# Kernel optimization log

Measured on AMD Instinct MI355X. Metric: run time of the kernel, lower is better.

Reference implementation:

```python
import jax, jax.numpy as jnp
import numpy as np

B = 2048        # patients (segments)
K = 4           # images per patient
C = 1280        # backbone_out (tf_efficientnet_b0)
PAIRS = K * (K - 1) // 2  # torch.combinations -> 6
NCLS = 1
N_DROP = 5


def setup_inputs() -> dict:
    key = jax.random.key(0)
    ks = jax.random.split(key, 8)
    x = jax.random.normal(ks[0], (B * K, C), jnp.float32)  # detached backbone features
    ids2 = jnp.repeat(jnp.arange(B, dtype=jnp.int32), PAIRS)  # segment id per pair
    Wc = jax.random.normal(ks[1], (C, C, 2), jnp.float32) * 0.02  # Conv1d(C,C,k=2) weight
    bc = jnp.zeros((C,), jnp.float32)
    W0 = jax.random.normal(ks[2], (NCLS, C), jnp.float32) * 0.02
    b0 = jnp.zeros((NCLS,), jnp.float32)
    W1 = jax.random.normal(ks[3], (1, C), jnp.float32) * 0.02
    b1 = jnp.zeros((1,), jnp.float32)
    W2 = jax.random.normal(ks[4], (1, C), jnp.float32) * 0.02
    b2 = jnp.zeros((1,), jnp.float32)
    return dict(x=x, ids2=ids2, Wc=Wc, bc=bc, W0=W0, b0=b0, W1=W1, b1=b1, W2=W2, b2=b2)


def reference(x, ids2, Wc, bc, W0, b0, W1, b1, W2, b2):
    # --- pair combinations within each patient group of K images ---
    ii, jj = np.triu_indices(K, 1)               # static [PAIRS]
    xg = x.reshape(B, K, C)
    xa = xg[:, ii].reshape(B * PAIRS, C)         # first element of each pair
    xb = xg[:, jj].reshape(B * PAIRS, C)         # second element
    # Conv1d(C, C, kernel=2) over the length-2 pair sequence + ReLU
    xc = jax.nn.relu(xa @ Wc[:, :, 0].T + xb @ Wc[:, :, 1].T + bc)  # [P, C]

    # --- 5 fixed dropout masks (p=0.5, train-mode scaling) ---
    masks = jax.random.bernoulli(jax.random.key(42), 0.5,
                                 (N_DROP, xc.shape[0], C)).astype(xc.dtype) * 2.0
    xd = xc[None] * masks                        # [D, P, C]

    cnt = jax.ops.segment_sum(jnp.ones_like(ids2, dtype=xc.dtype),
                              ids2, num_segments=B)  # [B], == PAIRS

    def agg(W, b):
        # head -> scalar mean over classes -> segment-mean over pairs -> mean over dropouts
        z = (jnp.einsum('dpc,oc->dpo', xd, W) + b).mean(-1)          # [D, P]
        s = jax.vmap(lambda u: jax.ops.segment_sum(u, ids2, num_segments=B))(z)
        return (s / cnt).mean(0)                                      # [B]

    logits = agg(W0, b0)
    logits1 = agg(W1, b1)
    logits2 = agg(W2, b2)
    return jnp.stack([logits, logits1, logits2], axis=1)  # [B, 3]
```

## Files before the change

kernel.cpp:

```cpp
#include <hip/hip_runtime.h>


typedef __attribute__((ext_vector_type(8))) short short8;
typedef __attribute__((ext_vector_type(4))) float f32x4;

#define PLANE 15728640u
#define KS2   (0x1BD11BDAu ^ 42u)

__device__ __forceinline__ unsigned short f2bf(float f) {
  unsigned int u = __builtin_bit_cast(unsigned int, f);
  u = (u + 0x7FFFu + ((u >> 16) & 1u)) >> 16;
  return (unsigned short)u;
}
__device__ __forceinline__ float bf2f(unsigned short h) {
  unsigned int u = ((unsigned int)h) << 16;
  return __builtin_bit_cast(float, u);
}

__global__ __launch_bounds__(256) void prep(
    const float* __restrict__ x, unsigned short* __restrict__ xb,
    const float* __restrict__ Wc, unsigned short* __restrict__ Wb,
    const float* __restrict__ b0, const float* __restrict__ b1,
    const float* __restrict__ b2, float* __restrict__ out) {
  const int bid = blockIdx.x;
  const int t = threadIdx.x;
  if (bid < 10240) {
    const int i = (bid * 256 + t) * 4;
    float4 v = *(const float4*)(x + i);
    ushort4 o;
    o.x = f2bf(v.x); o.y = f2bf(v.y); o.z = f2bf(v.z); o.w = f2bf(v.w);
    *(ushort4*)(xb + i) = o;
  } else if (bid < 23040) {
    const int idx = (bid - 10240) * 256 + t;
    const int n = idx / 2560;
    const int k = idx - n * 2560;
    const int side = (k >= 1280) ? 1 : 0;
    const int cin = k - side * 1280;
    Wb[idx] = f2bf(Wc[n * 2560 + cin * 2 + side]);
  } else {
    const int i = (bid - 23040) * 256 + t;
    if (i < 2048 * 3) {
      const int h = i % 3;
      out[i] = (h == 0) ? b0[0] : ((h == 1) ? b1[0] : b2[0]);
    }
  }
}

__device__ __forceinline__ unsigned int rotl(unsigned int x, int r) {
  return __builtin_amdgcn_alignbit(x, x, 32 - r);
}
__device__ __forceinline__ unsigned int tf_msb(unsigned int x1) {
  unsigned int x0 = x1;
  x1 = rotl(x1, 13) ^ x0;
#define TF_R(r) { x0 += x1; x1 = rotl(x1, (r)) ^ x0; }
  TF_R(15) TF_R(26) TF_R(6)
  x0 += 42u; x1 += KS2 + 1u;
  TF_R(17) TF_R(29) TF_R(16) TF_R(24)
  x0 += KS2; x1 += 2u;
  TF_R(13) TF_R(15) TF_R(26) TF_R(6)
  x1 += 42u + 3u;
  TF_R(17) TF_R(29) TF_R(16) TF_R(24)
  x0 += 42u; x1 += KS2 + 4u;
  TF_R(13) TF_R(15) TF_R(26) TF_R(6)
  x0 += KS2; x1 += 5u;
#undef TF_R
  return (x0 ^ x1) >> 31;
}

#define GL_LDS(g, l) __builtin_amdgcn_global_load_lds( \
    (const __attribute__((address_space(1))) unsigned int*)(g), \
    (__attribute__((address_space(3))) unsigned int*)(l), 16, 0, 0)

__global__ __launch_bounds__(256) void gemm_relu_dot(
    const unsigned short* __restrict__ Xb,
    const unsigned short* __restrict__ Wb,
    const float* __restrict__ bc,
    const float* __restrict__ W0, const float* __restrict__ W1,
    const float* __restrict__ W2, float* __restrict__ out)
{
  __shared__ unsigned short sA[2 * 128 * 32];
  __shared__ unsigned short sB[2 * 128 * 32];
  __shared__ unsigned int zLDS[8 * 256];
  __shared__ float rowsumA[128 * 3];
  __shared__ float rowsumB[128 * 3];

  const int t = threadIdx.x;
  const int mblk = blockIdx.x % 96;
  const int nblk = blockIdx.x / 96;
  const int p0 = mblk * 128, n0 = nblk * 128;
  const int lane = t & 63, w = t >> 6;
  const int wr = w >> 1, wc = w & 1;
  const int q = lane & 3;
  const int rl = lane >> 2;
  const int mrow = lane & 15;
  const int koff = (lane >> 4) * 8;
  const int mq = (lane >> 4) * 4;
  const int nn = lane & 15;

  int rA[2], rB[2], rN[2];
#pragma unroll
  for (int i = 0; i < 2; i++) {
    const int row = w * 32 + i * 16 + rl;
    const int pg = p0 + row;
    const int bA = pg / 6, pr = pg - bA * 6;
    rA[i] = bA * 4 + ((0x211000 >> (4 * pr)) & 7);
    rB[i] = bA * 4 + ((0x332321 >> (4 * pr)) & 7);
    rN[i] = n0 + row;
  }
  unsigned short* const ldsA0 = sA + (w * 32 + 0) * 32;
  unsigned short* const ldsA1 = sA + (w * 32 + 16) * 32;
  unsigned short* const ldsB0 = sB + (w * 32 + 0) * 32;
  unsigned short* const ldsB1 = sB + (w * 32 + 16) * 32;
  const unsigned short* const gA0s0 = Xb + rA[0] * 1280 + q * 8;
  const unsigned short* const gA1s0 = Xb + rA[1] * 1280 + q * 8;
  const unsigned short* const gA0s1 = Xb + rB[0] * 1280 + q * 8;
  const unsigned short* const gA1s1 = Xb + rB[1] * 1280 + q * 8;
  const unsigned short* const gB0 = Wb + rN[0] * 2560 + q * 8;
  const unsigned short* const gB1 = Wb + rN[1] * 2560 + q * 8;

  f32x4 acc[4][4];
#pragma unroll
  for (int i = 0; i < 4; i++)
#pragma unroll
    for (int j = 0; j < 4; j++) acc[i][j] = (f32x4){0.f, 0.f, 0.f, 0.f};

  const unsigned int tb =
      (unsigned int)((p0 + wr * 64 + mq) * 1280 + n0 + wc * 64 + nn) + 42u;

#define PF(nxt, bb)                                                          \
  {                                                                          \
    const int _n = (nxt);                                                    \
    if (_n < 80) {                                                           \
      const int _s1 = (_n >= 40);                                            \
      const unsigned short* _a0 = _s1 ? gA0s1 : gA0s0;                       \
      const unsigned short* _a1 = _s1 ? gA1s1 : gA1s0;                       \
      const int _kb = (_s1 ? (_n - 40) : _n) * 32;                           \
      const int _kg = _n * 32;                                               \
      GL_LDS(_a0 + _kb, ldsA0 + (bb) * 4096);                                \
      GL_LDS(_a1 + _kb, ldsA1 + (bb) * 4096);                                \
      GL_LDS(gB0 + _kg, ldsB0 + (bb) * 4096);                                \
      GL_LDS(gB1 + _kg, ldsB1 + (bb) * 4096);                                \
    }                                                                        \
  }

#define KSTEP(it, bb)                                                        \
  {                                                                          \
    __syncthreads();                                                         \
    short8 af[4], bfr[4];                                                    \
    _Pragma("unroll")                                                        \
    for (int i = 0; i < 4; i++)                                              \
      af[i] = *(const short8*)(sA + (bb) * 4096 +                            \
                               (wr * 64 + i * 16 + mrow) * 32 + koff);       \
    _Pragma("unroll")                                                        \
    for (int j = 0; j < 4; j++)                                              \
      bfr[j] = *(const short8*)(sB + (bb) * 4096 +                           \
                                (wc * 64 + j * 16 + mrow) * 32 + koff);      \
    PF((it) + 1, ((bb) ^ 1));                                                \
    _Pragma("unroll")                                                        \
    for (int i = 0; i < 4; i++)                                              \
      _Pragma("unroll")                                                      \
      for (int j = 0; j < 4; j++)                                            \
        acc[i][j] = __builtin_amdgcn_mfma_f32_16x16x32_bf16(af[i], bfr[j],   \
                                                            acc[i][j], 0, 0, 0); \
  }

#define CELL_RNG(it)                                                         \
  {                                                                          \
    const int idx = (it);                                                    \
    const unsigned int b = tb +                                              \
        (unsigned int)((((idx >> 4) * 16 + (idx & 3)) * 1280) +              \
                       (((idx >> 2) & 3) * 16));                             \
    const unsigned int z5 = tf_msb(b) + tf_msb(b + PLANE) +                  \
                            tf_msb(b + 2u * PLANE) + tf_msb(b + 3u * PLANE) +\
                            tf_msb(b + 4u * PLANE);                          \
    zacc |= z5 << (4 * sub);                                                 \
  }

  PF(0, 0);

  for (int c8 = 0; c8 < 8; c8++) {
    unsigned int zacc = 0;
#pragma unroll
    for (int sub = 0; sub < 8; sub++) {
      const int it = c8 * 8 + sub;
      KSTEP(it, (sub & 1));
      CELL_RNG(it);
    }
    zLDS[c8 * 256 + t] = zacc;
  }
  for (int c8 = 8; c8 < 10; c8++) {
#pragma unroll
    for (int sub = 0; sub < 8; sub++) {
      const int it = c8 * 8 + sub;
      KSTEP(it, (sub & 1));
    }
  }
#undef KSTEP
#undef PF
#undef CELL_RNG

  unsigned int zq[8];
#pragma unroll
  for (int c = 0; c < 8; c++) zq[c] = zLDS[c * 256 + t];

  float w0v[4], w1v[4], w2v[4], bcv[4];
#pragma unroll
  for (int j = 0; j < 4; j++) {
    const int n = n0 + wc * 64 + j * 16 + nn;
    w0v[j] = W0[n]; w1v[j] = W1[n]; w2v[j] = W2[n]; bcv[j] = bc[n];
  }

  float* const dst = (wc == 0) ? rowsumA : rowsumB;
#pragma unroll
  for (int i = 0; i < 4; i++) {
#pragma unroll
    for (int rg = 0; rg < 4; rg++) {
      float s0 = 0.f, s1 = 0.f, s2 = 0.f;
#pragma unroll
      for (int j = 0; j < 4; j++) {
        const int idx = i * 16 + j * 4 + rg;
        const unsigned int z5 = (zq[idx >> 3] >> (4 * (idx & 7))) & 7u;
        float v = acc[i][j][rg] + bcv[j];
        v = v > 0.f ? v : 0.f;
        const float tx = v * (float)(5 - (int)z5);
        s0 += tx * w0v[j]; s1 += tx * w1v[j]; s2 += tx * w2v[j];
      }
#pragma unroll
      for (int off = 1; off < 16; off <<= 1) {
        s0 += __shfl_xor(s0, off);
        s1 += __shfl_xor(s1, off);
        s2 += __shfl_xor(s2, off);
      }
      if (nn == 0) {
        const int row = wr * 64 + i * 16 + mq + rg;
        dst[row * 3 + 0] = s0; dst[row * 3 + 1] = s1; dst[row * 3 + 2] = s2;
      }
    }
  }
  __syncthreads();

  if (t < 128) {
    const int pr = p0 + t;
    const int rem = pr % 6;
    if (t == 0 || rem == 0) {
      int nrows = 6 - rem;
      if (nrows > 128 - t) nrows = 128 - t;
      float a0 = 0.f, a1 = 0.f, a2 = 0.f;
      for (int k2 = 0; k2 < nrows; k2++) {
        a0 += rowsumA[(t + k2) * 3 + 0] + rowsumB[(t + k2) * 3 + 0];
        a1 += rowsumA[(t + k2) * 3 + 1] + rowsumB[(t + k2) * 3 + 1];
        a2 += rowsumA[(t + k2) * 3 + 2] + rowsumB[(t + k2) * 3 + 2];
      }
      const int pat = pr / 6;
      atomicAdd(&out[pat * 3 + 0], a0 * (1.0f / 15.0f));
      atomicAdd(&out[pat * 3 + 1], a1 * (1.0f / 15.0f));
      atomicAdd(&out[pat * 3 + 2], a2 * (1.0f / 15.0f));
    }
  }
}

extern "C" void kernel_launch(void* const* d_in, const int* in_sizes, int n_in,
                              void* d_out, int out_size, void* d_ws, size_t ws_size,
                              hipStream_t stream) {
  const float* x  = (const float*)d_in[0];
  const float* Wc = (const float*)d_in[2];
  const float* bc = (const float*)d_in[3];
  const float* W0 = (const float*)d_in[4];
  const float* b0 = (const float*)d_in[5];
  const float* W1 = (const float*)d_in[6];
  const float* b1 = (const float*)d_in[7];
  const float* W2 = (const float*)d_in[8];
  const float* b2 = (const float*)d_in[9];
  float* out = (float*)d_out;

  char* ws = (char*)d_ws;
  unsigned short* xb = (unsigned short*)ws;
  unsigned short* Wb = (unsigned short*)(ws + 20971520);

  prep<<<23064, 256, 0, stream>>>(x, xb, Wc, Wb, b0, b1, b2, out);
  gemm_relu_dot<<<960, 256, 0, stream>>>(xb, Wb, bc, W0, W1, W2, out);
}
```

Before: 314.2 us.

## Halve GEMM N-tile, drop LDS double buffering, restructure Threefry rounds

Shrinks the N tile from 128 to 64, doubling the grid to 1920 blocks. Replaces the double-buffered async prefetch with a single-buffered load-sync-compute loop per k-step, and cuts LDS and accumulator registers. The Threefry MSB routine is rewritten with the key injections folded into the round adds. The aim is higher occupancy and better CU fill, at the cost of losing load/compute overlap, adding a second barrier per step and reusing the A tile less.

```diff
diff --git a/kernel.cpp b/kernel.cpp
--- a/kernel.cpp
+++ b/kernel.cpp
@@ -11,10 +11,6 @@
   unsigned int u = __builtin_bit_cast(unsigned int, f);
   u = (u + 0x7FFFu + ((u >> 16) & 1u)) >> 16;
   return (unsigned short)u;
-}
-__device__ __forceinline__ float bf2f(unsigned short h) {
-  unsigned int u = ((unsigned int)h) << 16;
-  return __builtin_bit_cast(float, u);
 }
 
 __global__ __launch_bounds__(256) void prep(
@@ -49,22 +45,30 @@
 __device__ __forceinline__ unsigned int rotl(unsigned int x, int r) {
   return __builtin_amdgcn_alignbit(x, x, 32 - r);
 }
-__device__ __forceinline__ unsigned int tf_msb(unsigned int x1) {
-  unsigned int x0 = x1;
-  x1 = rotl(x1, 13) ^ x0;
-#define TF_R(r) { x0 += x1; x1 = rotl(x1, (r)) ^ x0; }
-  TF_R(15) TF_R(26) TF_R(6)
-  x0 += 42u; x1 += KS2 + 1u;
-  TF_R(17) TF_R(29) TF_R(16) TF_R(24)
-  x0 += KS2; x1 += 2u;
-  TF_R(13) TF_R(15) TF_R(26) TF_R(6)
-  x1 += 42u + 3u;
-  TF_R(17) TF_R(29) TF_R(16) TF_R(24)
-  x0 += 42u; x1 += KS2 + 4u;
-  TF_R(13) TF_R(15) TF_R(26) TF_R(6)
-  x0 += KS2; x1 += 5u;
-#undef TF_R
-  return (x0 ^ x1) >> 31;
+__device__ __forceinline__ unsigned int tf_msb(unsigned int c) {
+  unsigned int x0 = c;
+  unsigned int x1 = rotl(c, 13) ^ c;
+  x0 += x1; x1 = rotl(x1, 15) ^ x0;
+  x0 += x1; x1 = rotl(x1, 26) ^ x0;
+  x0 += x1; x1 = rotl(x1, 6)  ^ x0;
+  unsigned int t;
+  t = x1 + (KS2 + 1u); x0 = x0 + t + 42u; x1 = rotl(t, 17) ^ x0;
+  x0 += x1; x1 = rotl(x1, 29) ^ x0;
+  x0 += x1; x1 = rotl(x1, 16) ^ x0;
+  x0 += x1; x1 = rotl(x1, 24) ^ x0;
+  t = x1 + 2u; x0 = x0 + t + KS2; x1 = rotl(t, 13) ^ x0;
+  x0 += x1; x1 = rotl(x1, 15) ^ x0;
+  x0 += x1; x1 = rotl(x1, 26) ^ x0;
+  x0 += x1; x1 = rotl(x1, 6)  ^ x0;
+  t = x1 + 45u; x0 = x0 + t; x1 = rotl(t, 17) ^ x0;
+  x0 += x1; x1 = rotl(x1, 29) ^ x0;
+  x0 += x1; x1 = rotl(x1, 16) ^ x0;
+  x0 += x1; x1 = rotl(x1, 24) ^ x0;
+  t = x1 + (KS2 + 4u); x0 = x0 + t + 42u; x1 = rotl(t, 13) ^ x0;
+  x0 += x1; x1 = rotl(x1, 15) ^ x0;
+  x0 += x1; x1 = rotl(x1, 26) ^ x0;
+  x0 += x1; x1 = rotl(x1, 6)  ^ x0;
+  return ((x0 + KS2) ^ (x1 + 5u)) >> 31;
 }
 
 #define GL_LDS(g, l) __builtin_amdgcn_global_load_lds( \
@@ -78,16 +82,17 @@
     const float* __restrict__ W0, const float* __restrict__ W1,
     const float* __restrict__ W2, float* __restrict__ out)
 {
-  __shared__ unsigned short sA[2 * 128 * 32];
-  __shared__ unsigned short sB[2 * 128 * 32];
-  __shared__ unsigned int zLDS[8 * 256];
+  __shared__ unsigned short sA[128 * 32];
+  __shared__ unsigned short sB[64 * 32];
+  __shared__ unsigned int zLDS[4 * 256];
   __shared__ float rowsumA[128 * 3];
   __shared__ float rowsumB[128 * 3];
 
   const int t = threadIdx.x;
-  const int mblk = blockIdx.x % 96;
-  const int nblk = blockIdx.x / 96;
-  const int p0 = mblk * 128, n0 = nblk * 128;
+  const int id = blockIdx.x;
+  const int mblk = id % 96;
+  const int nblk = id / 96;
+  const int p0 = mblk * 128, n0 = nblk * 64;
   const int lane = t & 63, w = t >> 6;
   const int wr = w >> 1, wc = w & 1;
   const int q = lane & 3;
@@ -97,7 +102,7 @@
   const int mq = (lane >> 4) * 4;
   const int nn = lane & 15;
 
-  int rA[2], rB[2], rN[2];
+  int rA[2], rB[2];
 #pragma unroll
   for (int i = 0; i < 2; i++) {
     const int row = w * 32 + i * 16 + rl;
@@ -105,61 +110,45 @@
     const int bA = pg / 6, pr = pg - bA * 6;
     rA[i] = bA * 4 + ((0x211000 >> (4 * pr)) & 7);
     rB[i] = bA * 4 + ((0x332321 >> (4 * pr)) & 7);
-    rN[i] = n0 + row;
-  }
+  }
+  const int rN = n0 + w * 16 + rl;
+
   unsigned short* const ldsA0 = sA + (w * 32 + 0) * 32;
   unsigned short* const ldsA1 = sA + (w * 32 + 16) * 32;
-  unsigned short* const ldsB0 = sB + (w * 32 + 0) * 32;
-  unsigned short* const ldsB1 = sB + (w * 32 + 16) * 32;
+  unsigned short* const ldsB0 = sB + (w * 16) * 32;
   const unsigned short* const gA0s0 = Xb + rA[0] * 1280 + q * 8;
   const unsigned short* const gA1s0 = Xb + rA[1] * 1280 + q * 8;
   const unsigned short* const gA0s1 = Xb + rB[0] * 1280 + q * 8;
   const unsigned short* const gA1s1 = Xb + rB[1] * 1280 + q * 8;
-  const unsigned short* const gB0 = Wb + rN[0] * 2560 + q * 8;
-  const unsigned short* const gB1 = Wb + rN[1] * 2560 + q * 8;
-
-  f32x4 acc[4][4];
+  const unsigned short* const gB0 = Wb + rN * 2560 + q * 8;
+
+  f32x4 acc[4][2];
 #pragma unroll
   for (int i = 0; i < 4; i++)
 #pragma unroll
-    for (int j = 0; j < 4; j++) acc[i][j] = (f32x4){0.f, 0.f, 0.f, 0.f};
+    for (int j = 0; j < 2; j++) acc[i][j] = (f32x4){0.f, 0.f, 0.f, 0.f};
 
   const unsigned int tb =
-      (unsigned int)((p0 + wr * 64 + mq) * 1280 + n0 + wc * 64 + nn) + 42u;
-
-#define PF(nxt, bb)                                                          \
-  {                                                                          \
-    const int _n = (nxt);                                                    \
-    if (_n < 80) {                                                           \
-      const int _s1 = (_n >= 40);                                            \
-      const unsigned short* _a0 = _s1 ? gA0s1 : gA0s0;                       \
-      const unsigned short* _a1 = _s1 ? gA1s1 : gA1s0;                       \
-      const int _kb = (_s1 ? (_n - 40) : _n) * 32;                           \
-      const int _kg = _n * 32;                                               \
-      GL_LDS(_a0 + _kb, ldsA0 + (bb) * 4096);                                \
-      GL_LDS(_a1 + _kb, ldsA1 + (bb) * 4096);                                \
-      GL_LDS(gB0 + _kg, ldsB0 + (bb) * 4096);                                \
-      GL_LDS(gB1 + _kg, ldsB1 + (bb) * 4096);                                \
-    }                                                                        \
-  }
-
-#define KSTEP(it, bb)                                                        \
+      (unsigned int)((p0 + wr * 64 + mq) * 1280 + n0 + wc * 32 + nn) + 42u;
+
+#define KSTEP(Ga0, Ga1, kb, kg)                                              \
   {                                                                          \
     __syncthreads();                                                         \
-    short8 af[4], bfr[4];                                                    \
+    GL_LDS(Ga0 + (kb), ldsA0);                                               \
+    GL_LDS(Ga1 + (kb), ldsA1);                                               \
+    GL_LDS(gB0 + (kg), ldsB0);                                               \
+    __syncthreads();                                                         \
+    short8 af[4], bfr[2];                                                    \
     _Pragma("unroll")                                                        \
     for (int i = 0; i < 4; i++)                                              \
-      af[i] = *(const short8*)(sA + (bb) * 4096 +                            \
-                               (wr * 64 + i * 16 + mrow) * 32 + koff);       \
+      af[i] = *(const short8*)(sA + (wr * 64 + i * 16 + mrow) * 32 + koff);  \
     _Pragma("unroll")                                                        \
-    for (int j = 0; j < 4; j++)                                              \
-      bfr[j] = *(const short8*)(sB + (bb) * 4096 +                           \
-                                (wc * 64 + j * 16 + mrow) * 32 + koff);      \
-    PF((it) + 1, ((bb) ^ 1));                                                \
+    for (int j = 0; j < 2; j++)                                              \
+      bfr[j] = *(const short8*)(sB + (wc * 32 + j * 16 + mrow) * 32 + koff); \
     _Pragma("unroll")                                                        \
     for (int i = 0; i < 4; i++)                                              \
       _Pragma("unroll")                                                      \
-      for (int j = 0; j < 4; j++)                                            \
+      for (int j = 0; j < 2; j++)                                            \
         acc[i][j] = __builtin_amdgcn_mfma_f32_16x16x32_bf16(af[i], bfr[j],   \
                                                             acc[i][j], 0, 0, 0); \
   }
@@ -168,45 +157,37 @@
   {                                                                          \
     const int idx = (it);                                                    \
     const unsigned int b = tb +                                              \
-        (unsigned int)((((idx >> 4) * 16 + (idx & 3)) * 1280) +              \
-                       (((idx >> 2) & 3) * 16));                             \
+        (unsigned int)((((idx >> 3) * 16 + (idx & 3)) * 1280) +              \
+                       (((idx >> 2) & 1) * 16));                             \
     const unsigned int z5 = tf_msb(b) + tf_msb(b + PLANE) +                  \
                             tf_msb(b + 2u * PLANE) + tf_msb(b + 3u * PLANE) +\
                             tf_msb(b + 4u * PLANE);                          \
     zacc |= z5 << (4 * sub);                                                 \
   }
 
-  PF(0, 0);
-
-  for (int c8 = 0; c8 < 8; c8++) {
+  for (int c8 = 0; c8 < 4; c8++) {
     unsigned int zacc = 0;
 #pragma unroll
     for (int sub = 0; sub < 8; sub++) {
       const int it = c8 * 8 + sub;
-      KSTEP(it, (sub & 1));
+      KSTEP(gA0s0, gA1s0, it * 32, it * 32);
       CELL_RNG(it);
     }
     zLDS[c8 * 256 + t] = zacc;
   }
-  for (int c8 = 8; c8 < 10; c8++) {
-#pragma unroll
-    for (int sub = 0; sub < 8; sub++) {
-      const int it = c8 * 8 + sub;
-      KSTEP(it, (sub & 1));
-    }
-  }
+  for (int it = 32; it < 40; it++) KSTEP(gA0s0, gA1s0, it * 32, it * 32);
+  for (int it = 40; it < 80; it++) KSTEP(gA0s1, gA1s1, (it - 40) * 32, it * 32);
 #undef KSTEP
-#undef PF
 #undef CELL_RNG
 
-  unsigned int zq[8];
-#pragma unroll
-  for (int c = 0; c < 8; c++) zq[c] = zLDS[c * 256 + t];
-
-  float w0v[4], w1v[4], w2v[4], bcv[4];
-#pragma unroll
-  for (int j = 0; j < 4; j++) {
-    const int n = n0 + wc * 64 + j * 16 + nn;
+  unsigned int zq[4];
+#pragma unroll
+  for (int c = 0; c < 4; c++) zq[c] = zLDS[c * 256 + t];
+
+  float w0v[2], w1v[2], w2v[2], bcv[2];
+#pragma unroll
+  for (int j = 0; j < 2; j++) {
+    const int n = n0 + wc * 32 + j * 16 + nn;
     w0v[j] = W0[n]; w1v[j] = W1[n]; w2v[j] = W2[n]; bcv[j] = bc[n];
   }
 
@@ -217,8 +198,8 @@
     for (int rg = 0; rg < 4; rg++) {
       float s0 = 0.f, s1 = 0.f, s2 = 0.f;
 #pragma unroll
-      for (int j = 0; j < 4; j++) {
-        const int idx = i * 16 + j * 4 + rg;
+      for (int j = 0; j < 2; j++) {
+        const int idx = i * 8 + j * 4 + rg;
         const unsigned int z5 = (zq[idx >> 3] >> (4 * (idx & 7))) & 7u;
         float v = acc[i][j][rg] + bcv[j];
         v = v > 0.f ? v : 0.f;
@@ -278,5 +259,5 @@
   unsigned short* Wb = (unsigned short*)(ws + 20971520);
 
   prep<<<23064, 256, 0, stream>>>(x, xb, Wc, Wb, b0, b1, b2, out);
-  gemm_relu_dot<<<960, 256, 0, stream>>>(xb, Wb, bc, W0, W1, W2, out);
-}
+  gemm_relu_dot<<<1920, 256, 0, stream>>>(xb, Wb, bc, W0, W1, W2, out);
+}
```

Result: no change. 314.0 us (-0.0%).
